# Performance work log

Measured on AMD Instinct MI355X. Metric: run time of the kernel, lower is better.

## Reference

```python
import jax, jax.numpy as jnp
import numpy as np

N_NODES = 40000
N_EDGES = 640000
IN_CH = 128
OUT_CH = 128
NUM_RBF = 64


def setup_inputs() -> dict:
    key = jax.random.key(0)
    ks = jax.random.split(key, 8)
    x = jax.random.normal(ks[0], (N_NODES, IN_CH), dtype=jnp.float32)
    edge_index = jax.random.randint(ks[1], (2, N_EDGES), 0, N_NODES, dtype=jnp.int64)
    edge_rbf = jax.random.uniform(ks[2], (N_EDGES, NUM_RBF), dtype=jnp.float32)
    s1 = 1.0 / np.sqrt(NUM_RBF)
    s2 = 1.0 / np.sqrt(OUT_CH)
    sl = 1.0 / np.sqrt(IN_CH)
    W1 = jax.random.normal(ks[3], (NUM_RBF, OUT_CH), dtype=jnp.float32) * s1
    b1 = jnp.zeros((OUT_CH,), dtype=jnp.float32)
    W2 = jax.random.normal(ks[4], (OUT_CH, OUT_CH), dtype=jnp.float32) * s2
    b2 = jnp.zeros((OUT_CH,), dtype=jnp.float32)
    Wl = jax.random.normal(ks[5], (IN_CH, OUT_CH), dtype=jnp.float32) * sl
    bl = jnp.zeros((OUT_CH,), dtype=jnp.float32)
    return {"x": x, "edge_index": edge_index, "edge_rbf": edge_rbf,
            "W1": W1, "b1": b1, "W2": W2, "b2": b2, "Wl": Wl, "bl": bl}


def reference(x, edge_index, edge_rbf, W1, b1, W2, b2, Wl, bl):
    # filter_net: Linear -> ReLU -> Linear on edge RBF features  [E, OUT_CH]
    weight = jnp.maximum(edge_rbf @ W1 + b1, 0.0) @ W2 + b2
    # node linear projection  [N, OUT_CH]
    h = x @ Wl + bl
    row, col = edge_index[0], edge_index[1]
    # gather source node features, modulate by continuous filter
    msg = h[col] * weight  # [E, OUT_CH]
    # scatter-sum messages onto destination nodes
    out = jax.ops.segment_sum(msg, row, num_segments=x.shape[0])
    return out
```

## Files before the change

kernel.cpp:

```cpp
#include <hip/hip_runtime.h>


#define N_NODES 40000
#define N_EDGES 640000
#define IN_CH 128
#define OUT_CH 128
#define NUM_RBF 64

#define TILE_M 64
#define NTILES (N_EDGES / TILE_M)
#define NB_NODE (N_NODES / TILE_M)
#define RBF_STR 72
#define T_STR 136
#define HV_STR 136
#define W_STR 72
#define W2_STR 136
#define NSCB ((N_NODES + 255) / 256)
#define EDGE_GRID 1280
#define K1_GRID 1024
#define ZC_BLOCKS 32
#define POOL_B 26880

typedef __attribute__((ext_vector_type(8))) short bf16x8;
typedef __attribute__((ext_vector_type(16))) float f32x16;

__device__ __forceinline__ unsigned short f2bf(float f) {
  unsigned u = __float_as_uint(f);
  return (unsigned short)((u + 0x7FFFu + ((u >> 16) & 1u)) >> 16);
}
__device__ __forceinline__ float bf2f(unsigned short s) {
  return __uint_as_float(((unsigned)s) << 16);
}

__global__ __launch_bounds__(256) void k1_kernel(
    const float* __restrict__ x, const float* __restrict__ Wl,
    const float* __restrict__ bl, unsigned short* __restrict__ hbf,
    int* __restrict__ count, float* __restrict__ outp) {
  __shared__ __align__(16) char pool[IN_CH * W2_STR * 2];
  const int bid = blockIdx.x;
  const int t = threadIdx.x;

  if (bid >= NB_NODE) {
    if (bid < NB_NODE + ZC_BLOCKS) {
      if (count) {
        int4 z = {0, 0, 0, 0};
        for (int i = (bid - NB_NODE) * 256 + t; i < N_NODES / 4;
             i += ZC_BLOCKS * 256)
          ((int4*)count)[i] = z;
      }
    } else {
      if (outp) {
        float4 z = {0.f, 0.f, 0.f, 0.f};
        const int nb = K1_GRID - NB_NODE - ZC_BLOCKS;
        for (int i = (bid - NB_NODE - ZC_BLOCKS) * 256 + t;
             i < N_NODES * OUT_CH / 4; i += nb * 256)
          ((float4*)outp)[i] = z;
      }
    }
    return;
  }

  const int lane = t & 63;
  const int l31 = lane & 31;
  const int lhalf = lane >> 5;
  const int wv = t >> 6;
  const int nbase = wv * 32 + l31;

  {
    unsigned short* sWT = (unsigned short*)pool;
    const int k2 = t >> 1;
    const int d0 = (t & 1) * 64;
#pragma unroll
    for (int i = 0; i < 16; ++i) {
      float4 v = *(const float4*)(Wl + k2 * OUT_CH + d0 + 4 * i);
      sWT[(d0 + 4 * i + 0) * W2_STR + k2] = f2bf(v.x);
      sWT[(d0 + 4 * i + 1) * W2_STR + k2] = f2bf(v.y);
      sWT[(d0 + 4 * i + 2) * W2_STR + k2] = f2bf(v.z);
      sWT[(d0 + 4 * i + 3) * W2_STR + k2] = f2bf(v.w);
    }
  }
  __syncthreads();
  bf16x8 BW[8];
  {
    const unsigned short* sWT = (const unsigned short*)pool;
#pragma unroll
    for (int kk = 0; kk < 8; ++kk)
      BW[kk] = *(const bf16x8*)&sWT[nbase * W2_STR + kk * 16 + lhalf * 8];
  }
  const float blv = bl[nbase];
  __syncthreads();

  const int rbase = bid * TILE_M;
  unsigned short* sX = (unsigned short*)pool;
  {
    const int m = t >> 2;
    const int c0 = (t & 3) * 32;
    const float* src = x + (size_t)(rbase + m) * IN_CH + c0;
#pragma unroll
    for (int i = 0; i < 8; ++i) {
      float4 v = *(const float4*)(src + 4 * i);
      ushort4 p;
      p.x = f2bf(v.x); p.y = f2bf(v.y); p.z = f2bf(v.z); p.w = f2bf(v.w);
      *(ushort4*)&sX[m * T_STR + c0 + 4 * i] = p;
    }
  }
  __syncthreads();
#pragma unroll
  for (int mt = 0; mt < 2; ++mt) {
    f32x16 acc = {0.f, 0.f, 0.f, 0.f, 0.f, 0.f, 0.f, 0.f,
                  0.f, 0.f, 0.f, 0.f, 0.f, 0.f, 0.f, 0.f};
#pragma unroll
    for (int kk = 0; kk < 8; ++kk) {
      bf16x8 A = *(const bf16x8*)&sX[(mt * 32 + l31) * T_STR + kk * 16 + lhalf * 8];
      acc = __builtin_amdgcn_mfma_f32_32x32x16_bf16(A, BW[kk], acc, 0, 0, 0);
    }
#pragma unroll
    for (int r = 0; r < 16; ++r) {
      const int rowm = mt * 32 + (r & 3) + 8 * (r >> 2) + 4 * lhalf;
      hbf[(size_t)(rbase + rowm) * OUT_CH + nbase] = f2bf(acc[r] + blv);
    }
  }
}

__global__ void hist_kernel(const int* __restrict__ rowI, int* __restrict__ count,
                            unsigned long long* __restrict__ status) {
  if (blockIdx.x == 0 && threadIdx.x < NSCB) status[threadIdx.x] = 0ULL;
  int e = blockIdx.x * 256 + threadIdx.x;
  if (e < N_EDGES) atomicAdd(&count[rowI[e]], 1);
}

__global__ __launch_bounds__(256) void scan_kernel(
    const int* __restrict__ count, unsigned long long* __restrict__ status,
    int* __restrict__ cursor) {
  __shared__ int s[256];
  __shared__ int wsum[4];
  const int t = threadIdx.x;
  const int b = blockIdx.x;
  const int i = b * 256 + t;
  const int v = (i < N_NODES) ? count[i] : 0;
  s[t] = v;
  __syncthreads();
  for (int off = 1; off < 256; off <<= 1) {
    int u = (t >= off) ? s[t - off] : 0;
    __syncthreads();
    s[t] += u;
    __syncthreads();
  }
  if (t == 255)
    __hip_atomic_store(&status[b], (1ULL << 32) | (unsigned)s[255],
                       __ATOMIC_RELEASE, __HIP_MEMORY_SCOPE_AGENT);
  int contrib = 0;
  if (t < b) {
    unsigned long long sv;
    do {
      sv = __hip_atomic_load(&status[t], __ATOMIC_ACQUIRE,
                             __HIP_MEMORY_SCOPE_AGENT);
    } while (!(sv >> 32));
    contrib = (int)(unsigned)sv;
  }
  for (int o = 32; o > 0; o >>= 1) contrib += __shfl_down(contrib, o, 64);
  if ((t & 63) == 0) wsum[t >> 6] = contrib;
  __syncthreads();
  const int boffv = wsum[0] + wsum[1] + wsum[2] + wsum[3];
  if (i < N_NODES) cursor[i] = boffv + s[t] - v;
}

__global__ void scatter_kernel(const int* __restrict__ rowI,
                               const int* __restrict__ colI,
                               int* __restrict__ cursor,
                               unsigned long long* __restrict__ packed) {
  int e = blockIdx.x * 256 + threadIdx.x;
  if (e < N_EDGES) {
    const int r = rowI[e];
    const int c = colI[e];
    const int p = atomicAdd(&cursor[r], 1);
    packed[p] = ((unsigned long long)r << 36) | ((unsigned long long)c << 20) |
                (unsigned)e;
  }
}

__global__ __launch_bounds__(256, 5) void edge_fused_kernel(
    const unsigned long long* __restrict__ packed, const float* __restrict__ rbf,
    const float* __restrict__ W1, const float* __restrict__ b1,
    const float* __restrict__ W2, const float* __restrict__ b2,
    const unsigned short* __restrict__ hbf, float* __restrict__ outp) {
  __shared__ __align__(16) char pool[POOL_B];

  unsigned short* sHv = (unsigned short*)pool;
  unsigned short* sT = (unsigned short*)pool;
  unsigned short* sRbf = (unsigned short*)(pool + TILE_M * HV_STR * 2);
  int* sAux = (int*)(pool + TILE_M * HV_STR * 2 + TILE_M * RBF_STR * 2);

  const int t = threadIdx.x;
  const int lane = t & 63;
  const int l31 = lane & 31;
  const int lhalf = lane >> 5;
  const int wv = t >> 6;
  const int nbase = wv * 32 + l31;

  unsigned short* sWT = (unsigned short*)pool;
  const int kst = t >> 2;
  const int dst0 = (t & 3) * 32;

  bf16x8 B1[4];
  bf16x8 B2[8];
  {
#pragma unroll
    for (int i = 0; i < 8; ++i) {
      float4 v = *(const float4*)(W1 + kst * OUT_CH + dst0 + 4 * i);
      sWT[(dst0 + 4 * i + 0) * W_STR + kst] = f2bf(v.x);
      sWT[(dst0 + 4 * i + 1) * W_STR + kst] = f2bf(v.y);
      sWT[(dst0 + 4 * i + 2) * W_STR + kst] = f2bf(v.z);
      sWT[(dst0 + 4 * i + 3) * W_STR + kst] = f2bf(v.w);
    }
    __syncthreads();
#pragma unroll
    for (int kk = 0; kk < 4; ++kk)
      B1[kk] = *(const bf16x8*)&sWT[nbase * W_STR + kk * 16 + lhalf * 8];
    __syncthreads();
#pragma unroll
    for (int i = 0; i < 8; ++i) {
      float4 v = *(const float4*)(W2 + kst * OUT_CH + dst0 + 4 * i);
      sWT[(dst0 + 4 * i + 0) * W_STR + kst] = f2bf(v.x);
      sWT[(dst0 + 4 * i + 1) * W_STR + kst] = f2bf(v.y);
      sWT[(dst0 + 4 * i + 2) * W_STR + kst] = f2bf(v.z);
      sWT[(dst0 + 4 * i + 3) * W_STR + kst] = f2bf(v.w);
    }
    __syncthreads();
#pragma unroll
    for (int kk = 0; kk < 4; ++kk)
      B2[kk] = *(const bf16x8*)&sWT[nbase * W_STR + kk * 16 + lhalf * 8];
    __syncthreads();
#pragma unroll
    for (int i = 0; i < 8; ++i) {
      float4 v = *(const float4*)(W2 + (64 + kst) * OUT_CH + dst0 + 4 * i);
      sWT[(dst0 + 4 * i + 0) * W_STR + kst] = f2bf(v.x);
      sWT[(dst0 + 4 * i + 1) * W_STR + kst] = f2bf(v.y);
      sWT[(dst0 + 4 * i + 2) * W_STR + kst] = f2bf(v.z);
      sWT[(dst0 + 4 * i + 3) * W_STR + kst] = f2bf(v.w);
    }
    __syncthreads();
#pragma unroll
    for (int kk = 0; kk < 4; ++kk)
      B2[4 + kk] = *(const bf16x8*)&sWT[nbase * W_STR + kk * 16 + lhalf * 8];
  }
  const float b1v = b1[nbase];
  const float b2v = b2[nbase];

  const int m4 = t >> 2;
  const int kq = (t & 3) * 16;

  for (int tile = blockIdx.x; tile < NTILES; tile += gridDim.x) {
    const int ebase = tile * TILE_M;
    __syncthreads();

    {
      const unsigned long long pkm = packed[ebase + m4];
      const float* src = rbf + (size_t)(pkm & 0xFFFFFu) * NUM_RBF + kq;
#pragma unroll
      for (int i = 0; i < 4; ++i) {
        float4 v = *(const float4*)(src + 4 * i);
        ushort4 p;
        p.x = f2bf(v.x); p.y = f2bf(v.y); p.z = f2bf(v.z); p.w = f2bf(v.w);
        *(ushort4*)&sRbf[m4 * RBF_STR + kq + 4 * i] = p;
      }
#pragma unroll
      for (int i = 0; i < 4; ++i) {
        const int chunk = t + 256 * i;
        const int row = chunk >> 4;
        const int c8 = (chunk & 15) * 8;
        const int col = (int)((packed[ebase + row] >> 20) & 0xFFFFu);
        *(uint4*)&sHv[row * HV_STR + c8] =
            *(const uint4*)(hbf + (size_t)col * OUT_CH + c8);
      }
      if (t < TILE_M) sAux[t] = (int)(packed[ebase + t] >> 36);
    }
    __syncthreads();

    float hv[2][16];
#pragma unroll
    for (int mt = 0; mt < 2; ++mt)
#pragma unroll
      for (int r = 0; r < 16; ++r) {
        const int rowm = mt * 32 + (r & 3) + 8 * (r >> 2) + 4 * lhalf;
        hv[mt][r] = bf2f(sHv[rowm * HV_STR + nbase]);
      }
    __syncthreads();

#pragma unroll
    for (int mt = 0; mt < 2; ++mt) {
      f32x16 acc = {0.f, 0.f, 0.f, 0.f, 0.f, 0.f, 0.f, 0.f,
                    0.f, 0.f, 0.f, 0.f, 0.f, 0.f, 0.f, 0.f};
#pragma unroll
      for (int kk = 0; kk < 4; ++kk) {
        bf16x8 A = *(const bf16x8*)&sRbf[(mt * 32 + l31) * RBF_STR + kk * 16 + lhalf * 8];
        acc = __builtin_amdgcn_mfma_f32_32x32x16_bf16(A, B1[kk], acc, 0, 0, 0);
      }
#pragma unroll
      for (int r = 0; r < 16; ++r) {
        const int rowm = (r & 3) + 8 * (r >> 2) + 4 * lhalf;
        float v = acc[r] + b1v;
        v = v > 0.f ? v : 0.f;
        sT[(mt * 32 + rowm) * T_STR + nbase] = f2bf(v);
      }
    }
    __syncthreads();

    float sum = 0.f;
    int curd = -1;
#pragma unroll
    for (int mt = 0; mt < 2; ++mt) {
      f32x16 acc = {0.f, 0.f, 0.f, 0.f, 0.f, 0.f, 0.f, 0.f,
                    0.f, 0.f, 0.f, 0.f, 0.f, 0.f, 0.f, 0.f};
#pragma unroll
      for (int kk = 0; kk < 8; ++kk) {
        bf16x8 A = *(const bf16x8*)&sT[(mt * 32 + l31) * T_STR + kk * 16 + lhalf * 8];
        acc = __builtin_amdgcn_mfma_f32_32x32x16_bf16(A, B2[kk], acc, 0, 0, 0);
      }
#pragma unroll
      for (int r = 0; r < 16; ++r) {
        const int rowm = mt * 32 + (r & 3) + 8 * (r >> 2) + 4 * lhalf;
        const float m = hv[mt][r] * (acc[r] + b2v);
        const int d = sAux[rowm];
        if (d != curd) {
          if (curd >= 0) atomicAdd(&outp[(size_t)curd * OUT_CH + nbase], sum);
          curd = d;
          sum = m;
        } else {
          sum += m;
        }
      }
    }
    atomicAdd(&outp[(size_t)curd * OUT_CH + nbase], sum);
  }
}

__global__ __launch_bounds__(256, 5) void edge_atomic_kernel(
    const int* __restrict__ eidx, const float* __restrict__ rbf,
    const float* __restrict__ W1, const float* __restrict__ b1,
    const float* __restrict__ W2, const float* __restrict__ b2,
    const unsigned short* __restrict__ hbf, float* __restrict__ outp) {
  __shared__ __align__(16) char pool[POOL_B];

  unsigned short* sHv = (unsigned short*)pool;
  unsigned short* sT = (unsigned short*)pool;
  unsigned short* sRbf = (unsigned short*)(pool + TILE_M * HV_STR * 2);
  int* sAux = (int*)(pool + TILE_M * HV_STR * 2 + TILE_M * RBF_STR * 2);

  const int t = threadIdx.x;
  const int lane = t & 63;
  const int l31 = lane & 31;
  const int lhalf = lane >> 5;
  const int wv = t >> 6;
  const int nbase = wv * 32 + l31;

  unsigned short* sWT = (unsigned short*)pool;
  const int kst = t >> 2;
  const int dst0 = (t & 3) * 32;

  bf16x8 B1[4];
  bf16x8 B2[8];
  {
#pragma unroll
    for (int i = 0; i < 8; ++i) {
      float4 v = *(const float4*)(W1 + kst * OUT_CH + dst0 + 4 * i);
      sWT[(dst0 + 4 * i + 0) * W_STR + kst] = f2bf(v.x);
      sWT[(dst0 + 4 * i + 1) * W_STR + kst] = f2bf(v.y);
      sWT[(dst0 + 4 * i + 2) * W_STR + kst] = f2bf(v.z);
      sWT[(dst0 + 4 * i + 3) * W_STR + kst] = f2bf(v.w);
    }
    __syncthreads();
#pragma unroll
    for (int kk = 0; kk < 4; ++kk)
      B1[kk] = *(const bf16x8*)&sWT[nbase * W_STR + kk * 16 + lhalf * 8];
    __syncthreads();
#pragma unroll
    for (int i = 0; i < 8; ++i) {
      float4 v = *(const float4*)(W2 + kst * OUT_CH + dst0 + 4 * i);
      sWT[(dst0 + 4 * i + 0) * W_STR + kst] = f2bf(v.x);
      sWT[(dst0 + 4 * i + 1) * W_STR + kst] = f2bf(v.y);
      sWT[(dst0 + 4 * i + 2) * W_STR + kst] = f2bf(v.z);
      sWT[(dst0 + 4 * i + 3) * W_STR + kst] = f2bf(v.w);
    }
    __syncthreads();
#pragma unroll
    for (int kk = 0; kk < 4; ++kk)
      B2[kk] = *(const bf16x8*)&sWT[nbase * W_STR + kk * 16 + lhalf * 8];
    __syncthreads();
#pragma unroll
    for (int i = 0; i < 8; ++i) {
      float4 v = *(const float4*)(W2 + (64 + kst) * OUT_CH + dst0 + 4 * i);
      sWT[(dst0 + 4 * i + 0) * W_STR + kst] = f2bf(v.x);
      sWT[(dst0 + 4 * i + 1) * W_STR + kst] = f2bf(v.y);
      sWT[(dst0 + 4 * i + 2) * W_STR + kst] = f2bf(v.z);
      sWT[(dst0 + 4 * i + 3) * W_STR + kst] = f2bf(v.w);
    }
    __syncthreads();
#pragma unroll
    for (int kk = 0; kk < 4; ++kk)
      B2[4 + kk] = *(const bf16x8*)&sWT[nbase * W_STR + kk * 16 + lhalf * 8];
  }
  const float b1v = b1[nbase];
  const float b2v = b2[nbase];

  const int* rowI = eidx;
  const int* colI = eidx + N_EDGES;

  for (int tile = blockIdx.x; tile < NTILES; tile += gridDim.x) {
    const int ebase = tile * TILE_M;
    __syncthreads();
    {
      const int m = t >> 2;
      const int kq = (t & 3) * 16;
      const float* src = rbf + (size_t)(ebase + m) * NUM_RBF + kq;
#pragma unroll
      for (int i = 0; i < 4; ++i) {
        float4 v = *(const float4*)(src + 4 * i);
        ushort4 p;
        p.x = f2bf(v.x); p.y = f2bf(v.y); p.z = f2bf(v.z); p.w = f2bf(v.w);
        *(ushort4*)&sRbf[m * RBF_STR + kq + 4 * i] = p;
      }
#pragma unroll
      for (int i = 0; i < 4; ++i) {
        const int chunk = t + 256 * i;
        const int row = chunk >> 4;
        const int c8 = (chunk & 15) * 8;
        const int col = colI[ebase + row];
        *(uint4*)&sHv[row * HV_STR + c8] =
            *(const uint4*)(hbf + (size_t)col * OUT_CH + c8);
      }
      if (t < TILE_M) sAux[t] = rowI[ebase + t];
    }
    __syncthreads();

    float hv[2][16];
#pragma unroll
    for (int mt = 0; mt < 2; ++mt)
#pragma unroll
      for (int r = 0; r < 16; ++r) {
        const int rowm = mt * 32 + (r & 3) + 8 * (r >> 2) + 4 * lhalf;
        hv[mt][r] = bf2f(sHv[rowm * HV_STR + nbase]);
      }
    __syncthreads();

#pragma unroll
    for (int mt = 0; mt < 2; ++mt) {
      f32x16 acc = {0.f, 0.f, 0.f, 0.f, 0.f, 0.f, 0.f, 0.f,
                    0.f, 0.f, 0.f, 0.f, 0.f, 0.f, 0.f, 0.f};
#pragma unroll
      for (int kk = 0; kk < 4; ++kk) {
        bf16x8 A = *(const bf16x8*)&sRbf[(mt * 32 + l31) * RBF_STR + kk * 16 + lhalf * 8];
        acc = __builtin_amdgcn_mfma_f32_32x32x16_bf16(A, B1[kk], acc, 0, 0, 0);
      }
#pragma unroll
      for (int r = 0; r < 16; ++r) {
        const int rowm = (r & 3) + 8 * (r >> 2) + 4 * lhalf;
        float v = acc[r] + b1v;
        v = v > 0.f ? v : 0.f;
        sT[(mt * 32 + rowm) * T_STR + nbase] = f2bf(v);
      }
    }
    __syncthreads();

    float sum = 0.f;
    int curd = -1;
#pragma unroll
    for (int mt = 0; mt < 2; ++mt) {
      f32x16 acc = {0.f, 0.f, 0.f, 0.f, 0.f, 0.f, 0.f, 0.f,
                    0.f, 0.f, 0.f, 0.f, 0.f, 0.f, 0.f, 0.f};
#pragma unroll
      for (int kk = 0; kk < 8; ++kk) {
        bf16x8 A = *(const bf16x8*)&sT[(mt * 32 + l31) * T_STR + kk * 16 + lhalf * 8];
        acc = __builtin_amdgcn_mfma_f32_32x32x16_bf16(A, B2[kk], acc, 0, 0, 0);
      }
#pragma unroll
      for (int r = 0; r < 16; ++r) {
        const int rowm = mt * 32 + (r & 3) + 8 * (r >> 2) + 4 * lhalf;
        const float m = hv[mt][r] * (acc[r] + b2v);
        const int d = sAux[rowm];
        if (d != curd) {
          if (curd >= 0) atomicAdd(&outp[(size_t)curd * OUT_CH + nbase], sum);
          curd = d;
          sum = m;
        } else {
          sum += m;
        }
      }
    }
    atomicAdd(&outp[(size_t)curd * OUT_CH + nbase], sum);
  }
}

extern "C" void kernel_launch(void* const* d_in, const int* in_sizes, int n_in,
                              void* d_out, int out_size, void* d_ws, size_t ws_size,
                              hipStream_t stream) {
  const float* x    = (const float*)d_in[0];
  const int*   eidx = (const int*)d_in[1];
  const float* rbf  = (const float*)d_in[2];
  const float* W1   = (const float*)d_in[3];
  const float* b1   = (const float*)d_in[4];
  const float* W2   = (const float*)d_in[5];
  const float* b2   = (const float*)d_in[6];
  const float* Wl   = (const float*)d_in[7];
  const float* bl   = (const float*)d_in[8];
  float* out = (float*)d_out;

  char* ws = (char*)d_ws;
  const size_t HBF_B = (size_t)N_NODES * OUT_CH * 2;
  const size_t PK_B = (size_t)N_EDGES * 8;
  const size_t CNT_B = (size_t)N_NODES * 4;
  const size_t ST_B = 1280;
  const size_t need = HBF_B + PK_B + 2 * CNT_B + ST_B + 64;

  size_t off = 0;
  unsigned short* hbf = (unsigned short*)(ws + off); off += HBF_B;
  unsigned long long* packed = (unsigned long long*)(ws + off); off += PK_B;
  int* count  = (int*)(ws + off); off += CNT_B;
  int* cursor = (int*)(ws + off); off += CNT_B;
  unsigned long long* status = (unsigned long long*)(ws + off); off += ST_B;

  const int* rowI = eidx;
  const int* colI = eidx + N_EDGES;

  if (ws_size >= need) {
    k1_kernel<<<K1_GRID, 256, 0, stream>>>(x, Wl, bl, hbf, count, out);
    hist_kernel<<<(N_EDGES + 255) / 256, 256, 0, stream>>>(rowI, count, status);
    scan_kernel<<<NSCB, 256, 0, stream>>>(count, status, cursor);
    scatter_kernel<<<(N_EDGES + 255) / 256, 256, 0, stream>>>(
        rowI, colI, cursor, packed);
    edge_fused_kernel<<<EDGE_GRID, 256, 0, stream>>>(
        packed, rbf, W1, b1, W2, b2, hbf, out);
  } else {
    hipMemsetAsync(out, 0, (size_t)N_NODES * OUT_CH * sizeof(float), stream);
    k1_kernel<<<NB_NODE, 256, 0, stream>>>(x, Wl, bl, hbf, nullptr, nullptr);
    edge_atomic_kernel<<<EDGE_GRID, 256, 0, stream>>>(
        eidx, rbf, W1, b1, W2, b2, hbf, out);
  }
}
```

Before: 496.8 us.

## Halve edge tile to 32 rows and fold histogram into node-projection kernel

The edge kernel now processes 32-edge tiles with a single MFMA row block per stage. That shrinks shared memory and drops one barrier per tile, at the cost of fewer rows per weight load and lower launch-bounds occupancy (4 instead of 5 blocks). The separate histogram kernel is removed: spare blocks of the node-projection kernel zero the output and then run the row-count atomics, and a memset clears count and status beforehand. This saves one launch but puts the atomic histogram in the same kernel that zeroes the output.

```diff
diff --git a/kernel.cpp b/kernel.cpp
--- a/kernel.cpp
+++ b/kernel.cpp
@@ -7,9 +7,9 @@
 #define OUT_CH 128
 #define NUM_RBF 64
 
-#define TILE_M 64
+#define TILE_M 32
 #define NTILES (N_EDGES / TILE_M)
-#define NB_NODE (N_NODES / TILE_M)
+#define NB_NODE (N_NODES / 64)
 #define RBF_STR 72
 #define T_STR 136
 #define HV_STR 136
@@ -18,8 +18,7 @@
 #define NSCB ((N_NODES + 255) / 256)
 #define EDGE_GRID 1280
 #define K1_GRID 1024
-#define ZC_BLOCKS 32
-#define POOL_B 26880
+#define POOL_B 18432
 
 typedef __attribute__((ext_vector_type(8))) short bf16x8;
 typedef __attribute__((ext_vector_type(16))) float f32x16;
@@ -35,27 +34,23 @@
 __global__ __launch_bounds__(256) void k1_kernel(
     const float* __restrict__ x, const float* __restrict__ Wl,
     const float* __restrict__ bl, unsigned short* __restrict__ hbf,
-    int* __restrict__ count, float* __restrict__ outp) {
+    const int* __restrict__ rowI, int* __restrict__ count,
+    float* __restrict__ outp) {
   __shared__ __align__(16) char pool[IN_CH * W2_STR * 2];
   const int bid = blockIdx.x;
   const int t = threadIdx.x;
 
   if (bid >= NB_NODE) {
-    if (bid < NB_NODE + ZC_BLOCKS) {
-      if (count) {
-        int4 z = {0, 0, 0, 0};
-        for (int i = (bid - NB_NODE) * 256 + t; i < N_NODES / 4;
-             i += ZC_BLOCKS * 256)
-          ((int4*)count)[i] = z;
-      }
-    } else {
-      if (outp) {
-        float4 z = {0.f, 0.f, 0.f, 0.f};
-        const int nb = K1_GRID - NB_NODE - ZC_BLOCKS;
-        for (int i = (bid - NB_NODE - ZC_BLOCKS) * 256 + t;
-             i < N_NODES * OUT_CH / 4; i += nb * 256)
-          ((float4*)outp)[i] = z;
-      }
+    const int nb = K1_GRID - NB_NODE;
+    if (outp) {
+      float4 z = {0.f, 0.f, 0.f, 0.f};
+      for (int i = (bid - NB_NODE) * 256 + t; i < N_NODES * OUT_CH / 4;
+           i += nb * 256)
+        ((float4*)outp)[i] = z;
+    }
+    if (count) {
+      for (int e = (bid - NB_NODE) * 256 + t; e < N_EDGES; e += nb * 256)
+        atomicAdd(&count[rowI[e]], 1);
     }
     return;
   }
@@ -90,7 +85,7 @@
   const float blv = bl[nbase];
   __syncthreads();
 
-  const int rbase = bid * TILE_M;
+  const int rbase = bid * 64;
   unsigned short* sX = (unsigned short*)pool;
   {
     const int m = t >> 2;
@@ -120,13 +115,6 @@
       hbf[(size_t)(rbase + rowm) * OUT_CH + nbase] = f2bf(acc[r] + blv);
     }
   }
-}
-
-__global__ void hist_kernel(const int* __restrict__ rowI, int* __restrict__ count,
-                            unsigned long long* __restrict__ status) {
-  if (blockIdx.x == 0 && threadIdx.x < NSCB) status[threadIdx.x] = 0ULL;
-  int e = blockIdx.x * 256 + threadIdx.x;
-  if (e < N_EDGES) atomicAdd(&count[rowI[e]], 1);
 }
 
 __global__ __launch_bounds__(256) void scan_kernel(
@@ -179,7 +167,7 @@
   }
 }
 
-__global__ __launch_bounds__(256, 5) void edge_fused_kernel(
+__global__ __launch_bounds__(256, 4) void edge_fused_kernel(
     const unsigned long long* __restrict__ packed, const float* __restrict__ rbf,
     const float* __restrict__ W1, const float* __restrict__ b1,
     const float* __restrict__ W2, const float* __restrict__ b2,
@@ -201,7 +189,6 @@
   unsigned short* sWT = (unsigned short*)pool;
   const int kst = t >> 2;
   const int dst0 = (t & 3) * 32;
-
   bf16x8 B1[4];
   bf16x8 B2[8];
   {
@@ -247,25 +234,25 @@
   const float b1v = b1[nbase];
   const float b2v = b2[nbase];
 
-  const int m4 = t >> 2;
-  const int kq = (t & 3) * 16;
+  const int m8 = t >> 3;
+  const int kq8 = (t & 7) * 8;
 
   for (int tile = blockIdx.x; tile < NTILES; tile += gridDim.x) {
     const int ebase = tile * TILE_M;
     __syncthreads();
 
     {
-      const unsigned long long pkm = packed[ebase + m4];
-      const float* src = rbf + (size_t)(pkm & 0xFFFFFu) * NUM_RBF + kq;
-#pragma unroll
-      for (int i = 0; i < 4; ++i) {
-        float4 v = *(const float4*)(src + 4 * i);
-        ushort4 p;
-        p.x = f2bf(v.x); p.y = f2bf(v.y); p.z = f2bf(v.z); p.w = f2bf(v.w);
-        *(ushort4*)&sRbf[m4 * RBF_STR + kq + 4 * i] = p;
-      }
-#pragma unroll
-      for (int i = 0; i < 4; ++i) {
+      const unsigned long long pkm = packed[ebase + m8];
+      const float* src = rbf + (size_t)(pkm & 0xFFFFFu) * NUM_RBF + kq8;
+      float4 v0 = *(const float4*)(src);
+      float4 v1 = *(const float4*)(src + 4);
+      ushort4 p;
+      p.x = f2bf(v0.x); p.y = f2bf(v0.y); p.z = f2bf(v0.z); p.w = f2bf(v0.w);
+      *(ushort4*)&sRbf[m8 * RBF_STR + kq8] = p;
+      p.x = f2bf(v1.x); p.y = f2bf(v1.y); p.z = f2bf(v1.z); p.w = f2bf(v1.w);
+      *(ushort4*)&sRbf[m8 * RBF_STR + kq8 + 4] = p;
+#pragma unroll
+      for (int i = 0; i < 2; ++i) {
         const int chunk = t + 256 * i;
         const int row = chunk >> 4;
         const int c8 = (chunk & 15) * 8;
@@ -277,23 +264,19 @@
     }
     __syncthreads();
 
-    float hv[2][16];
-#pragma unroll
-    for (int mt = 0; mt < 2; ++mt)
-#pragma unroll
-      for (int r = 0; r < 16; ++r) {
-        const int rowm = mt * 32 + (r & 3) + 8 * (r >> 2) + 4 * lhalf;
-        hv[mt][r] = bf2f(sHv[rowm * HV_STR + nbase]);
-      }
-    __syncthreads();
-
-#pragma unroll
-    for (int mt = 0; mt < 2; ++mt) {
+    float hv[16];
+#pragma unroll
+    for (int r = 0; r < 16; ++r) {
+      const int rowm = (r & 3) + 8 * (r >> 2) + 4 * lhalf;
+      hv[r] = bf2f(sHv[rowm * HV_STR + nbase]);
+    }
+
+    {
       f32x16 acc = {0.f, 0.f, 0.f, 0.f, 0.f, 0.f, 0.f, 0.f,
                     0.f, 0.f, 0.f, 0.f, 0.f, 0.f, 0.f, 0.f};
 #pragma unroll
       for (int kk = 0; kk < 4; ++kk) {
-        bf16x8 A = *(const bf16x8*)&sRbf[(mt * 32 + l31) * RBF_STR + kk * 16 + lhalf * 8];
+        bf16x8 A = *(const bf16x8*)&sRbf[l31 * RBF_STR + kk * 16 + lhalf * 8];
         acc = __builtin_amdgcn_mfma_f32_32x32x16_bf16(A, B1[kk], acc, 0, 0, 0);
       }
 #pragma unroll
@@ -301,26 +284,25 @@
         const int rowm = (r & 3) + 8 * (r >> 2) + 4 * lhalf;
         float v = acc[r] + b1v;
         v = v > 0.f ? v : 0.f;
-        sT[(mt * 32 + rowm) * T_STR + nbase] = f2bf(v);
-      }
-    }
-    __syncthreads();
-
-    float sum = 0.f;
-    int curd = -1;
-#pragma unroll
-    for (int mt = 0; mt < 2; ++mt) {
+        sT[rowm * T_STR + nbase] = f2bf(v);
+      }
+    }
+    __syncthreads();
+
+    {
       f32x16 acc = {0.f, 0.f, 0.f, 0.f, 0.f, 0.f, 0.f, 0.f,
                     0.f, 0.f, 0.f, 0.f, 0.f, 0.f, 0.f, 0.f};
 #pragma unroll
       for (int kk = 0; kk < 8; ++kk) {
-        bf16x8 A = *(const bf16x8*)&sT[(mt * 32 + l31) * T_STR + kk * 16 + lhalf * 8];
+        bf16x8 A = *(const bf16x8*)&sT[l31 * T_STR + kk * 16 + lhalf * 8];
         acc = __builtin_amdgcn_mfma_f32_32x32x16_bf16(A, B2[kk], acc, 0, 0, 0);
       }
+      float sum = 0.f;
+      int curd = -1;
 #pragma unroll
       for (int r = 0; r < 16; ++r) {
-        const int rowm = mt * 32 + (r & 3) + 8 * (r >> 2) + 4 * lhalf;
-        const float m = hv[mt][r] * (acc[r] + b2v);
+        const int rowm = (r & 3) + 8 * (r >> 2) + 4 * lhalf;
+        const float m = hv[r] * (acc[r] + b2v);
         const int d = sAux[rowm];
         if (d != curd) {
           if (curd >= 0) atomicAdd(&outp[(size_t)curd * OUT_CH + nbase], sum);
@@ -330,12 +312,12 @@
           sum += m;
         }
       }
-    }
-    atomicAdd(&outp[(size_t)curd * OUT_CH + nbase], sum);
-  }
-}
-
-__global__ __launch_bounds__(256, 5) void edge_atomic_kernel(
+      atomicAdd(&outp[(size_t)curd * OUT_CH + nbase], sum);
+    }
+  }
+}
+
+__global__ __launch_bounds__(256, 4) void edge_atomic_kernel(
     const int* __restrict__ eidx, const float* __restrict__ rbf,
     const float* __restrict__ W1, const float* __restrict__ b1,
     const float* __restrict__ W2, const float* __restrict__ b2,
@@ -357,7 +339,6 @@
   unsigned short* sWT = (unsigned short*)pool;
   const int kst = t >> 2;
   const int dst0 = (t & 3) * 32;
-
   bf16x8 B1[4];
   bf16x8 B2[8];
   {
@@ -405,23 +386,23 @@
 
   const int* rowI = eidx;
   const int* colI = eidx + N_EDGES;
+  const int m8 = t >> 3;
+  const int kq8 = (t & 7) * 8;
 
   for (int tile = blockIdx.x; tile < NTILES; tile += gridDim.x) {
     const int ebase = tile * TILE_M;
     __syncthreads();
     {
-      const int m = t >> 2;
-      const int kq = (t & 3) * 16;
-      const float* src = rbf + (size_t)(ebase + m) * NUM_RBF + kq;
-#pragma unroll
-      for (int i = 0; i < 4; ++i) {
-        float4 v = *(const float4*)(src + 4 * i);
-        ushort4 p;
-        p.x = f2bf(v.x); p.y = f2bf(v.y); p.z = f2bf(v.z); p.w = f2bf(v.w);
-        *(ushort4*)&sRbf[m * RBF_STR + kq + 4 * i] = p;
-      }
-#pragma unroll
-      for (int i = 0; i < 4; ++i) {
+      const float* src = rbf + (size_t)(ebase + m8) * NUM_RBF + kq8;
+      float4 v0 = *(const float4*)(src);
+      float4 v1 = *(const float4*)(src + 4);
+      ushort4 p;
+      p.x = f2bf(v0.x); p.y = f2bf(v0.y); p.z = f2bf(v0.z); p.w = f2bf(v0.w);
+      *(ushort4*)&sRbf[m8 * RBF_STR + kq8] = p;
+      p.x = f2bf(v1.x); p.y = f2bf(v1.y); p.z = f2bf(v1.z); p.w = f2bf(v1.w);
+      *(ushort4*)&sRbf[m8 * RBF_STR + kq8 + 4] = p;
+#pragma unroll
+      for (int i = 0; i < 2; ++i) {
         const int chunk = t + 256 * i;
         const int row = chunk >> 4;
         const int c8 = (chunk & 15) * 8;
@@ -433,23 +414,19 @@
     }
     __syncthreads();
 
-    float hv[2][16];
-#pragma unroll
-    for (int mt = 0; mt < 2; ++mt)
-#pragma unroll
-      for (int r = 0; r < 16; ++r) {
-        const int rowm = mt * 32 + (r & 3) + 8 * (r >> 2) + 4 * lhalf;
-        hv[mt][r] = bf2f(sHv[rowm * HV_STR + nbase]);
-      }
-    __syncthreads();
-
-#pragma unroll
-    for (int mt = 0; mt < 2; ++mt) {
+    float hv[16];
+#pragma unroll
+    for (int r = 0; r < 16; ++r) {
+      const int rowm = (r & 3) + 8 * (r >> 2) + 4 * lhalf;
+      hv[r] = bf2f(sHv[rowm * HV_STR + nbase]);
+    }
+
+    {
       f32x16 acc = {0.f, 0.f, 0.f, 0.f, 0.f, 0.f, 0.f, 0.f,
                     0.f, 0.f, 0.f, 0.f, 0.f, 0.f, 0.f, 0.f};
 #pragma unroll
       for (int kk = 0; kk < 4; ++kk) {
-        bf16x8 A = *(const bf16x8*)&sRbf[(mt * 32 + l31) * RBF_STR + kk * 16 + lhalf * 8];
+        bf16x8 A = *(const bf16x8*)&sRbf[l31 * RBF_STR + kk * 16 + lhalf * 8];
         acc = __builtin_amdgcn_mfma_f32_32x32x16_bf16(A, B1[kk], acc, 0, 0, 0);
       }
 #pragma unroll
@@ -457,26 +434,25 @@
         const int rowm = (r & 3) + 8 * (r >> 2) + 4 * lhalf;
         float v = acc[r] + b1v;
         v = v > 0.f ? v : 0.f;
-        sT[(mt * 32 + rowm) * T_STR + nbase] = f2bf(v);
-      }
-    }
-    __syncthreads();
-
-    float sum = 0.f;
-    int curd = -1;
-#pragma unroll
-    for (int mt = 0; mt < 2; ++mt) {
+        sT[rowm * T_STR + nbase] = f2bf(v);
+      }
+    }
+    __syncthreads();
+
+    {
       f32x16 acc = {0.f, 0.f, 0.f, 0.f, 0.f, 0.f, 0.f, 0.f,
                     0.f, 0.f, 0.f, 0.f, 0.f, 0.f, 0.f, 0.f};
 #pragma unroll
       for (int kk = 0; kk < 8; ++kk) {
-        bf16x8 A = *(const bf16x8*)&sT[(mt * 32 + l31) * T_STR + kk * 16 + lhalf * 8];
+        bf16x8 A = *(const bf16x8*)&sT[l31 * T_STR + kk * 16 + lhalf * 8];
         acc = __builtin_amdgcn_mfma_f32_32x32x16_bf16(A, B2[kk], acc, 0, 0, 0);
       }
+      float sum = 0.f;
+      int curd = -1;
 #pragma unroll
       for (int r = 0; r < 16; ++r) {
-        const int rowm = mt * 32 + (r & 3) + 8 * (r >> 2) + 4 * lhalf;
-        const float m = hv[mt][r] * (acc[r] + b2v);
+        const int rowm = (r & 3) + 8 * (r >> 2) + 4 * lhalf;
+        const float m = hv[r] * (acc[r] + b2v);
         const int d = sAux[rowm];
         if (d != curd) {
           if (curd >= 0) atomicAdd(&outp[(size_t)curd * OUT_CH + nbase], sum);
@@ -486,8 +462,8 @@
           sum += m;
         }
       }
-    }
-    atomicAdd(&outp[(size_t)curd * OUT_CH + nbase], sum);
+      atomicAdd(&outp[(size_t)curd * OUT_CH + nbase], sum);
+    }
   }
 }
 
@@ -510,21 +486,21 @@
   const size_t PK_B = (size_t)N_EDGES * 8;
   const size_t CNT_B = (size_t)N_NODES * 4;
   const size_t ST_B = 1280;
-  const size_t need = HBF_B + PK_B + 2 * CNT_B + ST_B + 64;
+  const size_t need = HBF_B + PK_B + CNT_B + ST_B + CNT_B + 64;
 
   size_t off = 0;
   unsigned short* hbf = (unsigned short*)(ws + off); off += HBF_B;
   unsigned long long* packed = (unsigned long long*)(ws + off); off += PK_B;
-  int* count  = (int*)(ws + off); off += CNT_B;
+  int* count = (int*)(ws + off); off += CNT_B;
+  unsigned long long* status = (unsigned long long*)(ws + off); off += ST_B;
   int* cursor = (int*)(ws + off); off += CNT_B;
-  unsigned long long* status = (unsigned long long*)(ws + off); off += ST_B;
 
   const int* rowI = eidx;
   const int* colI = eidx + N_EDGES;
 
   if (ws_size >= need) {
-    k1_kernel<<<K1_GRID, 256, 0, stream>>>(x, Wl, bl, hbf, count, out);
-    hist_kernel<<<(N_EDGES + 255) / 256, 256, 0, stream>>>(rowI, count, status);
+    hipMemsetAsync(count, 0, CNT_B + ST_B, stream);
+    k1_kernel<<<K1_GRID, 256, 0, stream>>>(x, Wl, bl, hbf, rowI, count, out);
     scan_kernel<<<NSCB, 256, 0, stream>>>(count, status, cursor);
     scatter_kernel<<<(N_EDGES + 255) / 256, 256, 0, stream>>>(
         rowI, colI, cursor, packed);
@@ -532,7 +508,8 @@
         packed, rbf, W1, b1, W2, b2, hbf, out);
   } else {
     hipMemsetAsync(out, 0, (size_t)N_NODES * OUT_CH * sizeof(float), stream);
-    k1_kernel<<<NB_NODE, 256, 0, stream>>>(x, Wl, bl, hbf, nullptr, nullptr);
+    k1_kernel<<<NB_NODE, 256, 0, stream>>>(x, Wl, bl, hbf, rowI, nullptr,
+                                           nullptr);
     edge_atomic_kernel<<<EDGE_GRID, 256, 0, stream>>>(
         eidx, rbf, W1, b1, W2, b2, hbf, out);
   }
```

Result: faster. 413.9 us (-16.7%).

## Fold edge histogram into node-projection kernel tail blocks and drop a barrier

Applied to the files above, without the earlier changes.

The separate histogram kernel is removed. The spare blocks of the node-projection kernel now zero the output and then atomically count destination rows. The count and status buffers are cleared with a single memset before launch, which saves one kernel launch and lets the histogram overlap the projection GEMM. A __syncthreads between the hv register reads and the sT writes is removed; this looks safe because each thread reads and writes only its own column. The edge kernels' launch bounds drop from 5 to 4 waves per SIMD, giving the compiler more registers at the cost of occupancy.

```diff
diff --git a/kernel.cpp b/kernel.cpp
--- a/kernel.cpp
+++ b/kernel.cpp
@@ -9,7 +9,7 @@
 
 #define TILE_M 64
 #define NTILES (N_EDGES / TILE_M)
-#define NB_NODE (N_NODES / TILE_M)
+#define NB_NODE (N_NODES / 64)
 #define RBF_STR 72
 #define T_STR 136
 #define HV_STR 136
@@ -18,7 +18,6 @@
 #define NSCB ((N_NODES + 255) / 256)
 #define EDGE_GRID 1280
 #define K1_GRID 1024
-#define ZC_BLOCKS 32
 #define POOL_B 26880
 
 typedef __attribute__((ext_vector_type(8))) short bf16x8;
@@ -35,27 +34,23 @@
 __global__ __launch_bounds__(256) void k1_kernel(
     const float* __restrict__ x, const float* __restrict__ Wl,
     const float* __restrict__ bl, unsigned short* __restrict__ hbf,
-    int* __restrict__ count, float* __restrict__ outp) {
+    const int* __restrict__ rowI, int* __restrict__ count,
+    float* __restrict__ outp) {
   __shared__ __align__(16) char pool[IN_CH * W2_STR * 2];
   const int bid = blockIdx.x;
   const int t = threadIdx.x;
 
   if (bid >= NB_NODE) {
-    if (bid < NB_NODE + ZC_BLOCKS) {
-      if (count) {
-        int4 z = {0, 0, 0, 0};
-        for (int i = (bid - NB_NODE) * 256 + t; i < N_NODES / 4;
-             i += ZC_BLOCKS * 256)
-          ((int4*)count)[i] = z;
-      }
-    } else {
-      if (outp) {
-        float4 z = {0.f, 0.f, 0.f, 0.f};
-        const int nb = K1_GRID - NB_NODE - ZC_BLOCKS;
-        for (int i = (bid - NB_NODE - ZC_BLOCKS) * 256 + t;
-             i < N_NODES * OUT_CH / 4; i += nb * 256)
-          ((float4*)outp)[i] = z;
-      }
+    const int nb = K1_GRID - NB_NODE;
+    if (outp) {
+      float4 z = {0.f, 0.f, 0.f, 0.f};
+      for (int i = (bid - NB_NODE) * 256 + t; i < N_NODES * OUT_CH / 4;
+           i += nb * 256)
+        ((float4*)outp)[i] = z;
+    }
+    if (count) {
+      for (int e = (bid - NB_NODE) * 256 + t; e < N_EDGES; e += nb * 256)
+        atomicAdd(&count[rowI[e]], 1);
     }
     return;
   }
@@ -90,7 +85,7 @@
   const float blv = bl[nbase];
   __syncthreads();
 
-  const int rbase = bid * TILE_M;
+  const int rbase = bid * 64;
   unsigned short* sX = (unsigned short*)pool;
   {
     const int m = t >> 2;
@@ -120,13 +115,6 @@
       hbf[(size_t)(rbase + rowm) * OUT_CH + nbase] = f2bf(acc[r] + blv);
     }
   }
-}
-
-__global__ void hist_kernel(const int* __restrict__ rowI, int* __restrict__ count,
-                            unsigned long long* __restrict__ status) {
-  if (blockIdx.x == 0 && threadIdx.x < NSCB) status[threadIdx.x] = 0ULL;
-  int e = blockIdx.x * 256 + threadIdx.x;
-  if (e < N_EDGES) atomicAdd(&count[rowI[e]], 1);
 }
 
 __global__ __launch_bounds__(256) void scan_kernel(
@@ -179,7 +167,7 @@
   }
 }
 
-__global__ __launch_bounds__(256, 5) void edge_fused_kernel(
+__global__ __launch_bounds__(256, 4) void edge_fused_kernel(
     const unsigned long long* __restrict__ packed, const float* __restrict__ rbf,
     const float* __restrict__ W1, const float* __restrict__ b1,
     const float* __restrict__ W2, const float* __restrict__ b2,
@@ -201,7 +189,6 @@
   unsigned short* sWT = (unsigned short*)pool;
   const int kst = t >> 2;
   const int dst0 = (t & 3) * 32;
-
   bf16x8 B1[4];
   bf16x8 B2[8];
   {
@@ -285,7 +272,6 @@
         const int rowm = mt * 32 + (r & 3) + 8 * (r >> 2) + 4 * lhalf;
         hv[mt][r] = bf2f(sHv[rowm * HV_STR + nbase]);
       }
-    __syncthreads();
 
 #pragma unroll
     for (int mt = 0; mt < 2; ++mt) {
@@ -335,7 +321,7 @@
   }
 }
 
-__global__ __launch_bounds__(256, 5) void edge_atomic_kernel(
+__global__ __launch_bounds__(256, 4) void edge_atomic_kernel(
     const int* __restrict__ eidx, const float* __restrict__ rbf,
     const float* __restrict__ W1, const float* __restrict__ b1,
     const float* __restrict__ W2, const float* __restrict__ b2,
@@ -357,7 +343,6 @@
   unsigned short* sWT = (unsigned short*)pool;
   const int kst = t >> 2;
   const int dst0 = (t & 3) * 32;
-
   bf16x8 B1[4];
   bf16x8 B2[8];
   {
@@ -405,20 +390,20 @@
 
   const int* rowI = eidx;
   const int* colI = eidx + N_EDGES;
+  const int m4 = t >> 2;
+  const int kq = (t & 3) * 16;
 
   for (int tile = blockIdx.x; tile < NTILES; tile += gridDim.x) {
     const int ebase = tile * TILE_M;
     __syncthreads();
     {
-      const int m = t >> 2;
-      const int kq = (t & 3) * 16;
-      const float* src = rbf + (size_t)(ebase + m) * NUM_RBF + kq;
+      const float* src = rbf + (size_t)(ebase + m4) * NUM_RBF + kq;
 #pragma unroll
       for (int i = 0; i < 4; ++i) {
         float4 v = *(const float4*)(src + 4 * i);
         ushort4 p;
         p.x = f2bf(v.x); p.y = f2bf(v.y); p.z = f2bf(v.z); p.w = f2bf(v.w);
-        *(ushort4*)&sRbf[m * RBF_STR + kq + 4 * i] = p;
+        *(ushort4*)&sRbf[m4 * RBF_STR + kq + 4 * i] = p;
       }
 #pragma unroll
       for (int i = 0; i < 4; ++i) {
@@ -441,7 +426,6 @@
         const int rowm = mt * 32 + (r & 3) + 8 * (r >> 2) + 4 * lhalf;
         hv[mt][r] = bf2f(sHv[rowm * HV_STR + nbase]);
       }
-    __syncthreads();
 
 #pragma unroll
     for (int mt = 0; mt < 2; ++mt) {
@@ -510,21 +494,21 @@
   const size_t PK_B = (size_t)N_EDGES * 8;
   const size_t CNT_B = (size_t)N_NODES * 4;
   const size_t ST_B = 1280;
-  const size_t need = HBF_B + PK_B + 2 * CNT_B + ST_B + 64;
+  const size_t need = HBF_B + PK_B + CNT_B + ST_B + CNT_B + 64;
 
   size_t off = 0;
   unsigned short* hbf = (unsigned short*)(ws + off); off += HBF_B;
   unsigned long long* packed = (unsigned long long*)(ws + off); off += PK_B;
-  int* count  = (int*)(ws + off); off += CNT_B;
+  int* count = (int*)(ws + off); off += CNT_B;
+  unsigned long long* status = (unsigned long long*)(ws + off); off += ST_B;
   int* cursor = (int*)(ws + off); off += CNT_B;
-  unsigned long long* status = (unsigned long long*)(ws + off); off += ST_B;
 
   const int* rowI = eidx;
   const int* colI = eidx + N_EDGES;
 
   if (ws_size >= need) {
-    k1_kernel<<<K1_GRID, 256, 0, stream>>>(x, Wl, bl, hbf, count, out);
-    hist_kernel<<<(N_EDGES + 255) / 256, 256, 0, stream>>>(rowI, count, status);
+    hipMemsetAsync(count, 0, CNT_B + ST_B, stream);
+    k1_kernel<<<K1_GRID, 256, 0, stream>>>(x, Wl, bl, hbf, rowI, count, out);
     scan_kernel<<<NSCB, 256, 0, stream>>>(count, status, cursor);
     scatter_kernel<<<(N_EDGES + 255) / 256, 256, 0, stream>>>(
         rowI, colI, cursor, packed);
@@ -532,7 +516,8 @@
         packed, rbf, W1, b1, W2, b2, hbf, out);
   } else {
     hipMemsetAsync(out, 0, (size_t)N_NODES * OUT_CH * sizeof(float), stream);
-    k1_kernel<<<NB_NODE, 256, 0, stream>>>(x, Wl, bl, hbf, nullptr, nullptr);
+    k1_kernel<<<NB_NODE, 256, 0, stream>>>(x, Wl, bl, hbf, rowI, nullptr,
+                                           nullptr);
     edge_atomic_kernel<<<EDGE_GRID, 256, 0, stream>>>(
         eidx, rbf, W1, b1, W2, b2, hbf, out);
   }
```

Measured after the change: 400.2 us. 19.4% less time.
